# Kernel optimization log

Measured on AMD Instinct MI355X. Metric: run time of the kernel, lower is better.

## Reference

```python
import jax, jax.numpy as jnp
import numpy as np

B, C, H, W = 8, 512, 64, 64
TEMB = 512
HIDDEN = 1024  # int(C * prompt_hidden_ratio=2.0)
K = C // 2     # max(1, int(C * topk_ratio=0.5))


def silu(x):
    return x * jax.nn.sigmoid(x)


def conv1x1(h, w, b):
    # h: [b,c,hh,ww], w: [out,in], b: [out]
    return jnp.einsum('bchw,oc->bohw', h, w) + b[None, :, None, None]


def setup_inputs() -> dict:
    key = jax.random.key(0)
    ks = jax.random.split(key, 12)
    s = 0.02  # small init so softmax/attention stay well-conditioned
    return {
        'x': jax.random.normal(ks[0], (B, C, H, W), jnp.float32),
        'temb': jax.random.normal(ks[1], (B, TEMB), jnp.float32),
        'w_affine': jax.random.normal(ks[2], (2 * C, TEMB), jnp.float32) * s,
        'b_affine': jnp.zeros((2 * C,), jnp.float32),
        'w_tp': jax.random.normal(ks[3], (C, TEMB), jnp.float32) * s,
        'b_tp': jnp.zeros((C,), jnp.float32),
        'w_m1': jax.random.normal(ks[4], (HIDDEN, 2 * C), jnp.float32) * s,
        'b_m1': jnp.zeros((HIDDEN,), jnp.float32),
        'w_m2': jax.random.normal(ks[5], (C, HIDDEN), jnp.float32) * s,
        'b_m2': jnp.zeros((C,), jnp.float32),
        'wq': jax.random.normal(ks[6], (C, C), jnp.float32) * s,
        'bq': jnp.zeros((C,), jnp.float32),
        'wk': jax.random.normal(ks[7], (C, C), jnp.float32) * s,
        'bk': jnp.zeros((C,), jnp.float32),
        'wv': jax.random.normal(ks[8], (C, C), jnp.float32) * s,
        'bv': jnp.zeros((C,), jnp.float32),
        'wo': jax.random.normal(ks[9], (C, C), jnp.float32) * s,
        'bo': jnp.zeros((C,), jnp.float32),
    }


def reference(x, temb, w_affine, b_affine, w_tp, b_tp, w_m1, b_m1, w_m2, b_m2,
              wq, bq, wk, bk, wv, bv, wo, bo):
    b, c, hgt, wgt = x.shape
    hw = hgt * wgt

    # TimeScaleShift
    temb_act = silu(temb)
    ss = temb_act @ w_affine.T + b_affine              # [b, 2c]
    scale, shift = jnp.split(ss, 2, axis=1)
    h = x * (1.0 + scale[:, :, None, None]) + shift[:, :, None, None]

    # channel prompt
    gap = h.mean(axis=(2, 3))                          # [b, c]
    time_prompt = temb_act @ w_tp.T + b_tp             # [b, c]
    pm = jnp.concatenate([gap, time_prompt], axis=1)   # [b, 2c]
    prompt = silu(pm @ w_m1.T + b_m1) @ w_m2.T + b_m2  # [b, c]

    # top-k channel selection
    _, topk_idx = jax.lax.top_k(prompt, K)             # [b, K] int32

    # q/k/v 1x1 convs, then gather selected channels
    qf = conv1x1(h, wq, bq).reshape(b, c, hw)
    kf = conv1x1(h, wk, bk).reshape(b, c, hw)
    vf = conv1x1(h, wv, bv).reshape(b, c, hw)
    idx3 = topk_idx[:, :, None]
    q = jnp.take_along_axis(qf, idx3, axis=1)          # [b, K, hw]
    k_feat = jnp.take_along_axis(kf, idx3, axis=1)
    v = jnp.take_along_axis(vf, idx3, axis=1)

    # channel attention on the selected subset
    attn = jnp.einsum('bkn,bln->bkl', q, k_feat) * (K ** -0.5)  # [b, K, K]
    attn = jax.nn.softmax(attn, axis=2)
    out = jnp.einsum('bkl,bln->bkn', attn, v)                   # [b, K, hw]

    # scatter back into a zero tensor at the selected channels
    out_full = jax.vmap(
        lambda o, i: jnp.zeros((c, hw), o.dtype).at[i].set(o)
    )(out, topk_idx).reshape(b, c, hgt, wgt)

    return conv1x1(out_full, wo, bo)
```

## Files before the change

### kernel.cpp

```cpp
#include <hip/hip_runtime.h>
#include <hip/hip_bf16.h>
#include <math.h>

typedef __hip_bfloat16 bf16;
typedef __bf16 bf16x8 __attribute__((ext_vector_type(8)));
typedef float f32x4 __attribute__((ext_vector_type(4)));

static __device__ __forceinline__ float b2f(bf16 v) { return __bfloat162float(v); }
static __device__ __forceinline__ bf16 f2b(float v) { return __float2bfloat16(v); }

#define TM 128
#define TN 64
#define TK 32

template <typename TOUT>
__global__ __launch_bounds__(256) void gemm_bt(
    const bf16* __restrict__ A, size_t sA,
    const bf16* __restrict__ Bt, size_t sB,
    const float* __restrict__ bias, size_t sBias, int hasBias,
    TOUT* __restrict__ D, size_t sD,
    int M, int N, int Kd, int transStore)
{
    A  += (size_t)blockIdx.z * sA;
    Bt += (size_t)blockIdx.z * sB;
    D  += (size_t)blockIdx.z * sD;
    if (hasBias) bias += (size_t)blockIdx.z * sBias;

    const int m0 = blockIdx.y * TM, n0 = blockIdx.x * TN;
    const int t = threadIdx.x, wv = t >> 6, lane = t & 63;
    const int lr = lane & 15, quad = lane >> 4;

    __shared__ bf16 lA[TM][TK + 8];
    __shared__ bf16 lB[TN][TK + 8];

    f32x4 acc[2][4];
#pragma unroll
    for (int i = 0; i < 2; ++i)
#pragma unroll
        for (int j = 0; j < 4; ++j) acc[i][j] = (f32x4){0.f, 0.f, 0.f, 0.f};

    const int arow = t >> 1, acol = (t & 1) * 16;
    const int brow = t >> 2, bcol = (t & 3) * 8;
    const bf16* aptr = A  + (size_t)(m0 + arow) * Kd + acol;
    const bf16* bptr = Bt + (size_t)(n0 + brow) * Kd + bcol;

    for (int k0 = 0; k0 < Kd; k0 += TK) {
        __syncthreads();
        uint4 a0 = *(const uint4*)(aptr + k0);
        uint4 a1 = *(const uint4*)(aptr + k0 + 8);
        uint4 b0 = *(const uint4*)(bptr + k0);
        *(uint4*)(&lA[arow][acol])     = a0;
        *(uint4*)(&lA[arow][acol + 8]) = a1;
        *(uint4*)(&lB[brow][bcol])     = b0;
        __syncthreads();

        bf16x8 af0 = *(const bf16x8*)(&lA[wv * 32 + lr][quad * 8]);
        bf16x8 af1 = *(const bf16x8*)(&lA[wv * 32 + 16 + lr][quad * 8]);
#pragma unroll
        for (int j = 0; j < 4; ++j) {
            bf16x8 bfj = *(const bf16x8*)(&lB[j * 16 + lr][quad * 8]);
            acc[0][j] = __builtin_amdgcn_mfma_f32_16x16x32_bf16(af0, bfj, acc[0][j], 0, 0, 0);
            acc[1][j] = __builtin_amdgcn_mfma_f32_16x16x32_bf16(af1, bfj, acc[1][j], 0, 0, 0);
        }
    }

#pragma unroll
    for (int i = 0; i < 2; ++i) {
        const int mb = m0 + wv * 32 + i * 16 + quad * 4;
#pragma unroll
        for (int r = 0; r < 4; ++r) {
            const int mm = mb + r;
            const float bvv = hasBias ? bias[mm] : 0.f;
#pragma unroll
            for (int j = 0; j < 4; ++j) {
                const int nn = n0 + j * 16 + lr;
                const float v = acc[i][j][r] + bvv;
                const size_t o = transStore ? ((size_t)nn * M + mm)
                                            : ((size_t)mm * N + nn);
                if constexpr (__is_same(TOUT, float)) D[o] = v;
                else                                  D[o] = f2b(v);
            }
        }
    }
}

#define BROW 40

__global__ __launch_bounds__(256) void gemm_qkv(
    const bf16* __restrict__ Aall, const float* __restrict__ x,
    const float* __restrict__ ss, const float* __restrict__ bias,
    bf16* __restrict__ qb, bf16* __restrict__ kb, bf16* __restrict__ vT)
{
    const int b = blockIdx.z;
    const int m0 = blockIdx.y * 128;
    const int n0 = blockIdx.x * 64;
    const bf16* A = Aall + (size_t)b * 393216;
    bias += b * 768;

    const int t = threadIdx.x, wv = t >> 6, lane = t & 63;
    const int lr = lane & 15, quad = lane >> 4;

    __shared__ bf16 lA[3][128][TK + 8];
    __shared__ bf16 lBf[64 * BROW];

    f32x4 acc[3][2][4];
#pragma unroll
    for (int m = 0; m < 3; ++m)
#pragma unroll
        for (int i = 0; i < 2; ++i)
#pragma unroll
            for (int j = 0; j < 4; ++j) acc[m][i][j] = (f32x4){0.f, 0.f, 0.f, 0.f};

    const int arow = t >> 1, acol = (t & 1) * 16;
    const bf16* aptr = A + (size_t)(m0 + arow) * 512 + acol;
    const int kk = t >> 3;
    const int w8 = kk >> 3;
    const int nc = (t & 7) * 8;
    const float* xp0 = x + ((size_t)b * 512 + kk) * 4096 + n0 + nc;
    const float* ssp = ss + b * 1024 + kk;

    for (int k0 = 0; k0 < 512; k0 += TK) {
        __syncthreads();
        uint4 a[3][2];
#pragma unroll
        for (int m = 0; m < 3; ++m) {
            a[m][0] = *(const uint4*)(aptr + m * 131072 + k0);
            a[m][1] = *(const uint4*)(aptr + m * 131072 + k0 + 8);
        }
        const float4 f0 = *(const float4*)(xp0 + (size_t)k0 * 4096);
        const float4 f1 = *(const float4*)(xp0 + (size_t)k0 * 4096 + 4);
        const float sc = 1.f + ssp[k0];
        const float sh = ssp[512 + k0];
#pragma unroll
        for (int m = 0; m < 3; ++m) {
            *(uint4*)(&lA[m][arow][acol])     = a[m][0];
            *(uint4*)(&lA[m][arow][acol + 8]) = a[m][1];
        }
        {
            const float vals[8] = {f0.x, f0.y, f0.z, f0.w, f1.x, f1.y, f1.z, f1.w};
#pragma unroll
            for (int i = 0; i < 8; ++i) {
                const int n = nc + i;
                lBf[n * BROW + ((w8 ^ ((n >> 3) & 3)) << 3) + (kk & 7)] =
                    f2b(fmaf(vals[i], sc, sh));
            }
        }
        __syncthreads();

        bf16x8 af[3][2];
#pragma unroll
        for (int m = 0; m < 3; ++m) {
            af[m][0] = *(const bf16x8*)(&lA[m][wv * 32 + lr][quad * 8]);
            af[m][1] = *(const bf16x8*)(&lA[m][wv * 32 + 16 + lr][quad * 8]);
        }
#pragma unroll
        for (int j = 0; j < 4; ++j) {
            const int n = j * 16 + lr;
            bf16x8 bfj = *(const bf16x8*)(&lBf[n * BROW + ((quad ^ ((n >> 3) & 3)) << 3)]);
#pragma unroll
            for (int m = 0; m < 3; ++m) {
                acc[m][0][j] = __builtin_amdgcn_mfma_f32_16x16x32_bf16(af[m][0], bfj, acc[m][0][j], 0, 0, 0);
                acc[m][1][j] = __builtin_amdgcn_mfma_f32_16x16x32_bf16(af[m][1], bfj, acc[m][1][j], 0, 0, 0);
            }
        }
    }

#pragma unroll
    for (int m = 0; m < 3; ++m) {
#pragma unroll
        for (int i = 0; i < 2; ++i) {
            const int mb = m0 + wv * 32 + i * 16 + quad * 4;
#pragma unroll
            for (int r = 0; r < 4; ++r) {
                const int mm = mb + r;
                const float bvv = bias[m * 256 + mm];
#pragma unroll
                for (int j = 0; j < 4; ++j) {
                    const int nn = n0 + j * 16 + lr;
                    const float v = acc[m][i][j][r] + bvv;
                    if (m == 0)      qb[(size_t)b * 1048576 + (size_t)mm * 4096 + nn] = f2b(v);
                    else if (m == 1) kb[(size_t)b * 1048576 + (size_t)mm * 4096 + nn] = f2b(v);
                    else             vT[(size_t)b * 1048576 + (size_t)nn * 256 + mm] = f2b(v);
                }
            }
        }
    }
}

__global__ __launch_bounds__(256) void gemm_s_splitk(
    const bf16* __restrict__ qb, const bf16* __restrict__ kb,
    float* __restrict__ part)
{
    const int b = blockIdx.z >> 4, s = blockIdx.z & 15;
    const int m0 = blockIdx.y * TM, n0 = blockIdx.x * TN;
    const bf16* A  = qb + (size_t)b * 1048576;
    const bf16* Bt = kb + (size_t)b * 1048576;

    const int t = threadIdx.x, wv = t >> 6, lane = t & 63;
    const int lr = lane & 15, quad = lane >> 4;

    __shared__ bf16 lA[TM][TK + 8];
    __shared__ bf16 lB[TN][TK + 8];

    f32x4 acc[2][4];
#pragma unroll
    for (int i = 0; i < 2; ++i)
#pragma unroll
        for (int j = 0; j < 4; ++j) acc[i][j] = (f32x4){0.f, 0.f, 0.f, 0.f};

    const int arow = t >> 1, acol = (t & 1) * 16;
    const int brow = t >> 2, bcol = (t & 3) * 8;
    const bf16* aptr = A  + (size_t)(m0 + arow) * 4096 + acol;
    const bf16* bptr = Bt + (size_t)(n0 + brow) * 4096 + bcol;

    const int kBeg = s * 256, kEnd = kBeg + 256;
    for (int k0 = kBeg; k0 < kEnd; k0 += TK) {
        __syncthreads();
        uint4 a0 = *(const uint4*)(aptr + k0);
        uint4 a1 = *(const uint4*)(aptr + k0 + 8);
        uint4 b0 = *(const uint4*)(bptr + k0);
        *(uint4*)(&lA[arow][acol])     = a0;
        *(uint4*)(&lA[arow][acol + 8]) = a1;
        *(uint4*)(&lB[brow][bcol])     = b0;
        __syncthreads();

        bf16x8 af0 = *(const bf16x8*)(&lA[wv * 32 + lr][quad * 8]);
        bf16x8 af1 = *(const bf16x8*)(&lA[wv * 32 + 16 + lr][quad * 8]);
#pragma unroll
        for (int j = 0; j < 4; ++j) {
            bf16x8 bfj = *(const bf16x8*)(&lB[j * 16 + lr][quad * 8]);
            acc[0][j] = __builtin_amdgcn_mfma_f32_16x16x32_bf16(af0, bfj, acc[0][j], 0, 0, 0);
            acc[1][j] = __builtin_amdgcn_mfma_f32_16x16x32_bf16(af1, bfj, acc[1][j], 0, 0, 0);
        }
    }

    float* dst = part + ((size_t)(s * 8 + b) * 256) * 256;
#pragma unroll
    for (int i = 0; i < 2; ++i) {
        const int mb = m0 + wv * 32 + i * 16 + quad * 4;
#pragma unroll
        for (int r = 0; r < 4; ++r) {
            const int mm = mb + r;
#pragma unroll
            for (int j = 0; j < 4; ++j)
                dst[(size_t)mm * 256 + n0 + j * 16 + lr] = acc[i][j][r];
        }
    }
}


__global__ void k_silu(const float* __restrict__ in, float* __restrict__ out, int n)
{
    int i = blockIdx.x * 256 + threadIdx.x;
    if (i < n) {
        float v = in[i];
        out[i] = v / (1.f + expf(-v));
    }
}

__global__ void k_xmean(const float* __restrict__ x, float* __restrict__ xsum)
{
    const int bc = blockIdx.x;
    const float4* p = (const float4*)(x + (size_t)bc * 4096);
    float s = 0.f;
#pragma unroll
    for (int r = 0; r < 4; ++r) {
        float4 v = p[threadIdx.x + r * 256];
        s += v.x + v.y + v.z + v.w;
    }
    for (int off = 32; off; off >>= 1) s += __shfl_down(s, off);
    __shared__ float red[4];
    if ((threadIdx.x & 63) == 0) red[threadIdx.x >> 6] = s;
    __syncthreads();
    if (threadIdx.x == 0)
        xsum[bc] = red[0] + red[1] + red[2] + red[3];
}

__global__ void k_smallgemm(const float* __restrict__ in, const float* __restrict__ W,
                            const float* __restrict__ bias, float* __restrict__ out,
                            int Mrows, int O, int Kd, int act)
{
    const int gw = (blockIdx.x * 256 + threadIdx.x) >> 6;
    const int lane = threadIdx.x & 63;
    if (gw >= Mrows * O) return;
    const int m = gw / O, o = gw - m * O;
    float s = 0.f;
    for (int k = lane; k < Kd; k += 64)
        s += in[m * Kd + k] * W[(size_t)o * Kd + k];
    for (int off = 32; off; off >>= 1) s += __shfl_down(s, off);
    if (lane == 0) {
        s += bias[o];
        if (act) s = s / (1.f + expf(-s));
        out[m * O + o] = s;
    }
}

__global__ void k_mlp1(const float* __restrict__ ss, const float* __restrict__ xsum,
                       const float* __restrict__ tp, const float* __restrict__ w_m1,
                       const float* __restrict__ b_m1, float* __restrict__ hidden)
{
    const int gw = (blockIdx.x * 256 + threadIdx.x) >> 6;
    const int lane = threadIdx.x & 63;
    if (gw >= 8 * 1024) return;
    const int m = gw >> 10, o = gw & 1023;
    float s = 0.f;
    for (int k = lane; k < 1024; k += 64) {
        float pv;
        if (k < 512) pv = (1.f + ss[m * 1024 + k]) * (xsum[m * 512 + k] * (1.f / 4096.f))
                          + ss[m * 1024 + 512 + k];
        else         pv = tp[m * 512 + k - 512];
        s += pv * w_m1[(size_t)o * 1024 + k];
    }
    for (int off = 32; off; off >>= 1) s += __shfl_down(s, off);
    if (lane == 0) {
        s += b_m1[o];
        hidden[m * 1024 + o] = s / (1.f + expf(-s));
    }
}

__global__ void k_topk(const float* __restrict__ prompt, int* __restrict__ idx)
{
    __shared__ float v[512];
    __shared__ int sel[512];
    const int b = blockIdx.x, c = threadIdx.x;
    v[c] = prompt[b * 512 + c];
    __syncthreads();
    const float mv = v[c];
    int rank = 0;
    for (int j = 0; j < 512; ++j) {
        float o = v[j];
        rank += (o > mv) || (o == mv && j < c);
    }
    sel[c] = (rank < 256) ? 1 : 0;
    __syncthreads();
    if (rank < 256) {
        int pos = 0;
        for (int j = 0; j < c; ++j) pos += sel[j];
        idx[b * 256 + pos] = c;
    }
}

__global__ void k_gather(const int* __restrict__ idx,
                         const float* __restrict__ wq, const float* __restrict__ bq,
                         const float* __restrict__ wk, const float* __restrict__ bk,
                         const float* __restrict__ wv, const float* __restrict__ bv,
                         const float* __restrict__ wo,
                         bf16* __restrict__ wqkv_g, float* __restrict__ bqkv_g,
                         bf16* __restrict__ wo_g)
{
    const int b = blockIdx.z;
    const int* id = idx + b * 256;
    const int tid = blockIdx.x * 256 + threadIdx.x;
    {
        const int mat = tid >> 17, r = tid & 131071;
        const int j = r >> 9, c = r & 511;
        const int ch = id[j];
        const float* W = mat == 0 ? wq : (mat == 1 ? wk : wv);
        wqkv_g[(size_t)b * 393216 + tid] = f2b(W[ch * 512 + c]);
    }
    if (tid < 131072) {
        const int o = tid >> 8, j = tid & 255;
        wo_g[(size_t)b * 131072 + tid] = f2b(wo[o * 512 + id[j]]);
    }
    if (tid < 768) {
        const int m2 = tid >> 8, j = tid & 255;
        const float* Bv = m2 == 0 ? bq : (m2 == 1 ? bk : bv);
        bqkv_g[b * 768 + tid] = Bv[id[j]];
    }
}

__global__ void k_softmax_red(const float* __restrict__ part, bf16* __restrict__ Pt)
{
    const int row = blockIdx.x;
    const int b = row >> 8, j = row & 255;
    const int t = threadIdx.x;
    const int lane = t & 63, wv = t >> 6;
    __shared__ float redm[4], reds[4];
    float v = 0.f;
#pragma unroll
    for (int s = 0; s < 16; ++s)
        v += part[((size_t)(s * 8 + b) * 256 + j) * 256 + t];
    v *= 0.0625f;
    float m = v;
    for (int off = 32; off; off >>= 1) m = fmaxf(m, __shfl_down(m, off));
    if (lane == 0) redm[wv] = m;
    __syncthreads();
    m = fmaxf(fmaxf(redm[0], redm[1]), fmaxf(redm[2], redm[3]));
    const float e = __expf(v - m);
    float s = e;
    for (int off = 32; off; off >>= 1) s += __shfl_down(s, off);
    if (lane == 0) reds[wv] = s;
    __syncthreads();
    s = reds[0] + reds[1] + reds[2] + reds[3];
    Pt[(size_t)b * 65536 + (size_t)t * 256 + j] = f2b(e / s);
}


extern "C" void kernel_launch(void* const* d_in, const int* in_sizes, int n_in,
                              void* d_out, int out_size, void* d_ws, size_t ws_size,
                              hipStream_t stream)
{
    const float* x        = (const float*)d_in[0];
    const float* temb     = (const float*)d_in[1];
    const float* w_affine = (const float*)d_in[2];
    const float* b_affine = (const float*)d_in[3];
    const float* w_tp     = (const float*)d_in[4];
    const float* b_tp     = (const float*)d_in[5];
    const float* w_m1     = (const float*)d_in[6];
    const float* b_m1     = (const float*)d_in[7];
    const float* w_m2     = (const float*)d_in[8];
    const float* b_m2     = (const float*)d_in[9];
    const float* wq       = (const float*)d_in[10];
    const float* bq       = (const float*)d_in[11];
    const float* wk       = (const float*)d_in[12];
    const float* bk       = (const float*)d_in[13];
    const float* wv       = (const float*)d_in[14];
    const float* bv       = (const float*)d_in[15];
    const float* wo       = (const float*)d_in[16];
    const float* bo       = (const float*)d_in[17];
    float* out = (float*)d_out;

    char* ws = (char*)d_ws;
    size_t off = 0;
    auto alloc = [&](size_t bytes) -> char* {
        char* p = ws + off;
        off += (bytes + 255) & ~(size_t)255;
        return p;
    };

    float* temb_act = (float*)alloc(4096 * 4);
    float* ssb      = (float*)alloc(8192 * 4);
    float* tp       = (float*)alloc(4096 * 4);
    float* xsum     = (float*)alloc(4096 * 4);
    float* hidden   = (float*)alloc(8192 * 4);
    float* prompt   = (float*)alloc(4096 * 4);
    int*   idx      = (int*)alloc(2048 * 4);
    float* part   = (float*)alloc((size_t)16 * 8 * 256 * 256 * 4);
    bf16*  wqkv_g = (bf16*)alloc((size_t)8 * 768 * 512 * 2);
    float* bqkv_g = (float*)alloc(8 * 768 * 4);
    bf16*  wo_g   = (bf16*)alloc((size_t)8 * 512 * 256 * 2);
    bf16*  qb     = (bf16*)alloc((size_t)8 * 256 * 4096 * 2);
    bf16*  kb     = (bf16*)alloc((size_t)8 * 256 * 4096 * 2);
    bf16*  vT     = (bf16*)alloc((size_t)8 * 4096 * 256 * 2);
    bf16*  Pt     = (bf16*)alloc((size_t)8 * 256 * 256 * 2);
    bf16*  W2     = (bf16*)alloc((size_t)8 * 512 * 256 * 2);
    (void)ws_size; (void)n_in; (void)in_sizes; (void)out_size;

    k_silu<<<16, 256, 0, stream>>>(temb, temb_act, 4096);
    k_xmean<<<4096, 256, 0, stream>>>(x, xsum);
    k_smallgemm<<<2048, 256, 0, stream>>>(temb_act, w_affine, b_affine, ssb, 8, 1024, 512, 0);
    k_smallgemm<<<1024, 256, 0, stream>>>(temb_act, w_tp, b_tp, tp, 8, 512, 512, 0);
    k_mlp1<<<2048, 256, 0, stream>>>(ssb, xsum, tp, w_m1, b_m1, hidden);
    k_smallgemm<<<1024, 256, 0, stream>>>(hidden, w_m2, b_m2, prompt, 8, 512, 1024, 0);
    k_topk<<<8, 512, 0, stream>>>(prompt, idx);
    k_gather<<<dim3(1536, 1, 8), 256, 0, stream>>>(idx, wq, bq, wk, bk, wv, bv, wo,
                                                   wqkv_g, bqkv_g, wo_g);
    gemm_qkv<<<dim3(64, 2, 8), 256, 0, stream>>>(wqkv_g, x, ssb, bqkv_g, qb, kb, vT);
    gemm_s_splitk<<<dim3(4, 2, 128), 256, 0, stream>>>(qb, kb, part);
    k_softmax_red<<<2048, 256, 0, stream>>>(part, Pt);
    gemm_bt<bf16><<<dim3(4, 4, 8), 256, 0, stream>>>(wo_g, 131072, Pt, 65536,
                                                     nullptr, 0, 0,
                                                     W2, 131072, 512, 256, 256, 0);
    gemm_bt<float><<<dim3(64, 4, 8), 256, 0, stream>>>(W2, 131072, vT, 1048576,
                                                       bo, 0, 1,
                                                       out, 2097152, 512, 4096, 256, 0);
}
```

Measured before the change: 333.3 us.

## Reformulate channel attention via Gram matrix of x and folded weight products

Replaces the explicit q/k/v projections over all 4096 pixels with algebraic reassociation. It computes the symmetric Gram matrix x·xᵀ once per batch (upper-triangular tiles only), applies the scale/shift correction analytically, and forms the attention scores as Wq·G·Wkᵀ using hi/lo bf16 splitting for accuracy. The output path folds Wo·P·Wv·diag(1+scale) into one 512x512 matrix applied directly to x, with the shift and biases folded into a per-channel bias. This removes the large q/k/v intermediates and their HBM traffic, at the cost of more small kernels and possible bf16 precision loss in the Gram and fused weights.

```diff
diff --git a/kernel.cpp b/kernel.cpp
--- a/kernel.cpp
+++ b/kernel.cpp
@@ -8,30 +8,38 @@
 
 static __device__ __forceinline__ float b2f(bf16 v) { return __bfloat162float(v); }
 static __device__ __forceinline__ bf16 f2b(float v) { return __float2bfloat16(v); }
-
-#define TM 128
-#define TN 64
+static __device__ __forceinline__ unsigned int packbf(float a, float b)
+{
+    bf16 ha = f2b(a), hb = f2b(b);
+    unsigned short ua, ub;
+    __builtin_memcpy(&ua, &ha, 2);
+    __builtin_memcpy(&ub, &hb, 2);
+    return (unsigned int)ua | ((unsigned int)ub << 16);
+}
+
 #define TK 32
 
 template <typename TOUT>
 __global__ __launch_bounds__(256) void gemm_bt(
     const bf16* __restrict__ A, size_t sA,
     const bf16* __restrict__ Bt, size_t sB,
-    const float* __restrict__ bias, size_t sBias, int hasBias,
+    const float* __restrict__ bias, size_t sBias,
+    const float* __restrict__ colScale, size_t sCS,
     TOUT* __restrict__ D, size_t sD,
     int M, int N, int Kd, int transStore)
 {
     A  += (size_t)blockIdx.z * sA;
     Bt += (size_t)blockIdx.z * sB;
     D  += (size_t)blockIdx.z * sD;
-    if (hasBias) bias += (size_t)blockIdx.z * sBias;
-
-    const int m0 = blockIdx.y * TM, n0 = blockIdx.x * TN;
+    if (bias)     bias     += (size_t)blockIdx.z * sBias;
+    if (colScale) colScale += (size_t)blockIdx.z * sCS;
+
+    const int m0 = blockIdx.y * 128, n0 = blockIdx.x * 64;
     const int t = threadIdx.x, wv = t >> 6, lane = t & 63;
     const int lr = lane & 15, quad = lane >> 4;
 
-    __shared__ bf16 lA[TM][TK + 8];
-    __shared__ bf16 lB[TN][TK + 8];
+    __shared__ bf16 lA[128][TK + 8];
+    __shared__ bf16 lB[64][TK + 8];
 
     f32x4 acc[2][4];
 #pragma unroll
@@ -70,11 +78,12 @@
 #pragma unroll
         for (int r = 0; r < 4; ++r) {
             const int mm = mb + r;
-            const float bvv = hasBias ? bias[mm] : 0.f;
+            const float bvv = bias ? bias[mm] : 0.f;
 #pragma unroll
             for (int j = 0; j < 4; ++j) {
                 const int nn = n0 + j * 16 + lr;
-                const float v = acc[i][j][r] + bvv;
+                float v = acc[i][j][r] + bvv;
+                if (colScale) v *= (1.f + colScale[nn]);
                 const size_t o = transStore ? ((size_t)nn * M + mm)
                                             : ((size_t)mm * N + nn);
                 if constexpr (__is_same(TOUT, float)) D[o] = v;
@@ -84,123 +93,113 @@
     }
 }
 
-#define BROW 40
-
-__global__ __launch_bounds__(256) void gemm_qkv(
-    const bf16* __restrict__ Aall, const float* __restrict__ x,
-    const float* __restrict__ ss, const float* __restrict__ bias,
-    bf16* __restrict__ qb, bf16* __restrict__ kb, bf16* __restrict__ vT)
-{
-    const int b = blockIdx.z;
-    const int m0 = blockIdx.y * 128;
-    const int n0 = blockIdx.x * 64;
-    const bf16* A = Aall + (size_t)b * 393216;
-    bias += b * 768;
-
+__global__ __launch_bounds__(256) void gemm_bt2(
+    const bf16* __restrict__ A1, const bf16* __restrict__ A2, size_t sA,
+    const bf16* __restrict__ B1, const bf16* __restrict__ B2, size_t sB,
+    bf16* __restrict__ Dhi, bf16* __restrict__ Dlo,
+    float* __restrict__ Df, size_t sD,
+    int M, int N, int Kd, int transStore)
+{
+    A1 += (size_t)blockIdx.z * sA;
+    A2 += (size_t)blockIdx.z * sA;
+    B1 += (size_t)blockIdx.z * sB;
+    B2 += (size_t)blockIdx.z * sB;
+
+    const int m0 = blockIdx.y * 128, n0 = blockIdx.x * 64;
     const int t = threadIdx.x, wv = t >> 6, lane = t & 63;
     const int lr = lane & 15, quad = lane >> 4;
 
-    __shared__ bf16 lA[3][128][TK + 8];
-    __shared__ bf16 lBf[64 * BROW];
-
-    f32x4 acc[3][2][4];
-#pragma unroll
-    for (int m = 0; m < 3; ++m)
-#pragma unroll
-        for (int i = 0; i < 2; ++i)
-#pragma unroll
-            for (int j = 0; j < 4; ++j) acc[m][i][j] = (f32x4){0.f, 0.f, 0.f, 0.f};
+    __shared__ bf16 lA1[128][TK + 8];
+    __shared__ bf16 lA2[128][TK + 8];
+    __shared__ bf16 lB1[64][TK + 8];
+    __shared__ bf16 lB2[64][TK + 8];
+
+    f32x4 acc[2][4];
+#pragma unroll
+    for (int i = 0; i < 2; ++i)
+#pragma unroll
+        for (int j = 0; j < 4; ++j) acc[i][j] = (f32x4){0.f, 0.f, 0.f, 0.f};
 
     const int arow = t >> 1, acol = (t & 1) * 16;
-    const bf16* aptr = A + (size_t)(m0 + arow) * 512 + acol;
-    const int kk = t >> 3;
-    const int w8 = kk >> 3;
-    const int nc = (t & 7) * 8;
-    const float* xp0 = x + ((size_t)b * 512 + kk) * 4096 + n0 + nc;
-    const float* ssp = ss + b * 1024 + kk;
-
-    for (int k0 = 0; k0 < 512; k0 += TK) {
-        __syncthreads();
-        uint4 a[3][2];
-#pragma unroll
-        for (int m = 0; m < 3; ++m) {
-            a[m][0] = *(const uint4*)(aptr + m * 131072 + k0);
-            a[m][1] = *(const uint4*)(aptr + m * 131072 + k0 + 8);
-        }
-        const float4 f0 = *(const float4*)(xp0 + (size_t)k0 * 4096);
-        const float4 f1 = *(const float4*)(xp0 + (size_t)k0 * 4096 + 4);
-        const float sc = 1.f + ssp[k0];
-        const float sh = ssp[512 + k0];
-#pragma unroll
-        for (int m = 0; m < 3; ++m) {
-            *(uint4*)(&lA[m][arow][acol])     = a[m][0];
-            *(uint4*)(&lA[m][arow][acol + 8]) = a[m][1];
-        }
-        {
-            const float vals[8] = {f0.x, f0.y, f0.z, f0.w, f1.x, f1.y, f1.z, f1.w};
-#pragma unroll
-            for (int i = 0; i < 8; ++i) {
-                const int n = nc + i;
-                lBf[n * BROW + ((w8 ^ ((n >> 3) & 3)) << 3) + (kk & 7)] =
-                    f2b(fmaf(vals[i], sc, sh));
-            }
-        }
-        __syncthreads();
-
-        bf16x8 af[3][2];
-#pragma unroll
-        for (int m = 0; m < 3; ++m) {
-            af[m][0] = *(const bf16x8*)(&lA[m][wv * 32 + lr][quad * 8]);
-            af[m][1] = *(const bf16x8*)(&lA[m][wv * 32 + 16 + lr][quad * 8]);
-        }
+    const int brow = t >> 2, bcol = (t & 3) * 8;
+    const size_t aoff = (size_t)(m0 + arow) * Kd + acol;
+    const size_t boff = (size_t)(n0 + brow) * Kd + bcol;
+
+    for (int k0 = 0; k0 < Kd; k0 += TK) {
+        __syncthreads();
+        uint4 a10 = *(const uint4*)(A1 + aoff + k0);
+        uint4 a11 = *(const uint4*)(A1 + aoff + k0 + 8);
+        uint4 a20 = *(const uint4*)(A2 + aoff + k0);
+        uint4 a21 = *(const uint4*)(A2 + aoff + k0 + 8);
+        uint4 b1  = *(const uint4*)(B1 + boff + k0);
+        uint4 b2  = *(const uint4*)(B2 + boff + k0);
+        *(uint4*)(&lA1[arow][acol])     = a10;
+        *(uint4*)(&lA1[arow][acol + 8]) = a11;
+        *(uint4*)(&lA2[arow][acol])     = a20;
+        *(uint4*)(&lA2[arow][acol + 8]) = a21;
+        *(uint4*)(&lB1[brow][bcol])     = b1;
+        *(uint4*)(&lB2[brow][bcol])     = b2;
+        __syncthreads();
+
+        bf16x8 a1f0 = *(const bf16x8*)(&lA1[wv * 32 + lr][quad * 8]);
+        bf16x8 a1f1 = *(const bf16x8*)(&lA1[wv * 32 + 16 + lr][quad * 8]);
+        bf16x8 a2f0 = *(const bf16x8*)(&lA2[wv * 32 + lr][quad * 8]);
+        bf16x8 a2f1 = *(const bf16x8*)(&lA2[wv * 32 + 16 + lr][quad * 8]);
 #pragma unroll
         for (int j = 0; j < 4; ++j) {
-            const int n = j * 16 + lr;
-            bf16x8 bfj = *(const bf16x8*)(&lBf[n * BROW + ((quad ^ ((n >> 3) & 3)) << 3)]);
-#pragma unroll
-            for (int m = 0; m < 3; ++m) {
-                acc[m][0][j] = __builtin_amdgcn_mfma_f32_16x16x32_bf16(af[m][0], bfj, acc[m][0][j], 0, 0, 0);
-                acc[m][1][j] = __builtin_amdgcn_mfma_f32_16x16x32_bf16(af[m][1], bfj, acc[m][1][j], 0, 0, 0);
-            }
-        }
-    }
-
-#pragma unroll
-    for (int m = 0; m < 3; ++m) {
-#pragma unroll
-        for (int i = 0; i < 2; ++i) {
-            const int mb = m0 + wv * 32 + i * 16 + quad * 4;
-#pragma unroll
-            for (int r = 0; r < 4; ++r) {
-                const int mm = mb + r;
-                const float bvv = bias[m * 256 + mm];
-#pragma unroll
-                for (int j = 0; j < 4; ++j) {
-                    const int nn = n0 + j * 16 + lr;
-                    const float v = acc[m][i][j][r] + bvv;
-                    if (m == 0)      qb[(size_t)b * 1048576 + (size_t)mm * 4096 + nn] = f2b(v);
-                    else if (m == 1) kb[(size_t)b * 1048576 + (size_t)mm * 4096 + nn] = f2b(v);
-                    else             vT[(size_t)b * 1048576 + (size_t)nn * 256 + mm] = f2b(v);
+            bf16x8 b1j = *(const bf16x8*)(&lB1[j * 16 + lr][quad * 8]);
+            bf16x8 b2j = *(const bf16x8*)(&lB2[j * 16 + lr][quad * 8]);
+            acc[0][j] = __builtin_amdgcn_mfma_f32_16x16x32_bf16(a1f0, b1j, acc[0][j], 0, 0, 0);
+            acc[0][j] = __builtin_amdgcn_mfma_f32_16x16x32_bf16(a2f0, b2j, acc[0][j], 0, 0, 0);
+            acc[1][j] = __builtin_amdgcn_mfma_f32_16x16x32_bf16(a1f1, b1j, acc[1][j], 0, 0, 0);
+            acc[1][j] = __builtin_amdgcn_mfma_f32_16x16x32_bf16(a2f1, b2j, acc[1][j], 0, 0, 0);
+        }
+    }
+
+#pragma unroll
+    for (int i = 0; i < 2; ++i) {
+        const int mb = m0 + wv * 32 + i * 16 + quad * 4;
+#pragma unroll
+        for (int r = 0; r < 4; ++r) {
+            const int mm = mb + r;
+#pragma unroll
+            for (int j = 0; j < 4; ++j) {
+                const int nn = n0 + j * 16 + lr;
+                const float v = acc[i][j][r];
+                const size_t o = (transStore ? ((size_t)nn * M + mm)
+                                             : ((size_t)mm * N + nn))
+                                 + (size_t)blockIdx.z * sD;
+                if (Df) {
+                    Df[o] = v;
+                } else {
+                    bf16 h = f2b(v);
+                    Dhi[o] = h;
+                    Dlo[o] = f2b(v - b2f(h));
                 }
             }
         }
     }
 }
 
-__global__ __launch_bounds__(256) void gemm_s_splitk(
-    const bf16* __restrict__ qb, const bf16* __restrict__ kb,
-    float* __restrict__ part)
-{
-    const int b = blockIdx.z >> 4, s = blockIdx.z & 15;
-    const int m0 = blockIdx.y * TM, n0 = blockIdx.x * TN;
-    const bf16* A  = qb + (size_t)b * 1048576;
-    const bf16* Bt = kb + (size_t)b * 1048576;
+__global__ __launch_bounds__(256) void gemm_gram(
+    const float* __restrict__ x, float* __restrict__ part)
+{
+    const int li = blockIdx.x, s = blockIdx.y, b = blockIdx.z;
+    int mi, ni;
+    if (li < 8)       { mi = 0; ni = li; }
+    else if (li < 14) { mi = 1; ni = li - 6; }
+    else if (li < 18) { mi = 2; ni = li - 10; }
+    else              { mi = 3; ni = li - 12; }
+    const int m0 = mi * 128, n0 = ni * 64;
+    const float* xb = x + (size_t)b * 512 * 4096;
 
     const int t = threadIdx.x, wv = t >> 6, lane = t & 63;
     const int lr = lane & 15, quad = lane >> 4;
 
-    __shared__ bf16 lA[TM][TK + 8];
-    __shared__ bf16 lB[TN][TK + 8];
+    __shared__ bf16 lA[128][TK + 8];
+    __shared__ bf16 lB[64][TK + 8];
+    unsigned int* lAu = (unsigned int*)lA;
+    unsigned int* lBu = (unsigned int*)lB;
 
     f32x4 acc[2][4];
 #pragma unroll
@@ -210,18 +209,30 @@
 
     const int arow = t >> 1, acol = (t & 1) * 16;
     const int brow = t >> 2, bcol = (t & 3) * 8;
-    const bf16* aptr = A  + (size_t)(m0 + arow) * 4096 + acol;
-    const bf16* bptr = Bt + (size_t)(n0 + brow) * 4096 + bcol;
-
-    const int kBeg = s * 256, kEnd = kBeg + 256;
+    const float* aptr = xb + (size_t)(m0 + arow) * 4096 + acol;
+    const float* bptr = xb + (size_t)(n0 + brow) * 4096 + bcol;
+
+    const int kBeg = s * 1024, kEnd = kBeg + 1024;
     for (int k0 = kBeg; k0 < kEnd; k0 += TK) {
         __syncthreads();
-        uint4 a0 = *(const uint4*)(aptr + k0);
-        uint4 a1 = *(const uint4*)(aptr + k0 + 8);
-        uint4 b0 = *(const uint4*)(bptr + k0);
-        *(uint4*)(&lA[arow][acol])     = a0;
-        *(uint4*)(&lA[arow][acol + 8]) = a1;
-        *(uint4*)(&lB[brow][bcol])     = b0;
+        float4 af[4], bf[2];
+#pragma unroll
+        for (int q = 0; q < 4; ++q) af[q] = *(const float4*)(aptr + k0 + q * 4);
+#pragma unroll
+        for (int q = 0; q < 2; ++q) bf[q] = *(const float4*)(bptr + k0 + q * 4);
+        {
+            unsigned int w[8];
+            const float* fa = (const float*)af;
+#pragma unroll
+            for (int q = 0; q < 8; ++q) w[q] = packbf(fa[2 * q], fa[2 * q + 1]);
+            *(uint4*)&lAu[arow * 20 + acol / 2]     = *(uint4*)&w[0];
+            *(uint4*)&lAu[arow * 20 + acol / 2 + 4] = *(uint4*)&w[4];
+            unsigned int v[4];
+            const float* fb = (const float*)bf;
+#pragma unroll
+            for (int q = 0; q < 4; ++q) v[q] = packbf(fb[2 * q], fb[2 * q + 1]);
+            *(uint4*)&lBu[brow * 20 + bcol / 2] = *(uint4*)&v[0];
+        }
         __syncthreads();
 
         bf16x8 af0 = *(const bf16x8*)(&lA[wv * 32 + lr][quad * 8]);
@@ -234,7 +245,7 @@
         }
     }
 
-    float* dst = part + ((size_t)(s * 8 + b) * 256) * 256;
+    float* dst = part + ((size_t)(s * 8 + b)) * 262144;
 #pragma unroll
     for (int i = 0; i < 2; ++i) {
         const int mb = m0 + wv * 32 + i * 16 + quad * 4;
@@ -243,7 +254,104 @@
             const int mm = mb + r;
 #pragma unroll
             for (int j = 0; j < 4; ++j)
-                dst[(size_t)mm * 256 + n0 + j * 16 + lr] = acc[i][j][r];
+                dst[(size_t)mm * 512 + n0 + j * 16 + lr] = acc[i][j][r];
+        }
+    }
+}
+
+__global__ void k_fixG(const float* __restrict__ part, const float* __restrict__ ss,
+                       const float* __restrict__ xsum,
+                       bf16* __restrict__ Ghi, bf16* __restrict__ Glo)
+{
+    const int e = blockIdx.x * 256 + threadIdx.x;
+    const int b = e >> 18, rem = e & 262143;
+    const int c1 = rem >> 9, c2 = rem & 511;
+    const int stored = (c2 >> 6) >= 2 * (c1 >> 7);
+    const size_t src = stored ? ((size_t)c1 * 512 + c2) : ((size_t)c2 * 512 + c1);
+    float gx = 0.f;
+#pragma unroll
+    for (int s = 0; s < 4; ++s)
+        gx += part[((size_t)(s * 8 + b)) * 262144 + src];
+    const float s1 = ss[b * 1024 + c1], sh1 = ss[b * 1024 + 512 + c1];
+    const float s2 = ss[b * 1024 + c2], sh2 = ss[b * 1024 + 512 + c2];
+    const float xs1 = xsum[b * 512 + c1], xs2 = xsum[b * 512 + c2];
+    const float g = (1.f + s1) * (1.f + s2) * gx + (1.f + s1) * sh2 * xs1
+                    + sh1 * (1.f + s2) * xs2 + 4096.f * sh1 * sh2;
+    const bf16 h = f2b(g);
+    Ghi[e] = h;
+    Glo[e] = f2b(g - b2f(h));
+}
+
+__global__ __launch_bounds__(256) void gemm_final(
+    const bf16* __restrict__ W3p, const float* __restrict__ x,
+    const float* __restrict__ bias2, float* __restrict__ out)
+{
+    const int b = blockIdx.z;
+    const int m0 = blockIdx.y * 128, n0 = blockIdx.x * 64;
+    const bf16* A = W3p + (size_t)b * 262144;
+    const float* xb = x + (size_t)b * 512 * 4096;
+    bias2 += b * 512;
+    out += (size_t)b * 2097152;
+
+    const int t = threadIdx.x, wv = t >> 6, lane = t & 63;
+    const int lr = lane & 15, quad = lane >> 4;
+
+    __shared__ bf16 lA[128][TK + 8];
+    __shared__ unsigned int lBu[64 * 20];
+
+    f32x4 acc[2][4];
+#pragma unroll
+    for (int i = 0; i < 2; ++i)
+#pragma unroll
+        for (int j = 0; j < 4; ++j) acc[i][j] = (f32x4){0.f, 0.f, 0.f, 0.f};
+
+    const int arow = t >> 1, acol = (t & 1) * 16;
+    const bf16* aptr = A + (size_t)(m0 + arow) * 512 + acol;
+    const int kp = t >> 4, nc = (t & 15) * 4;
+    const int grp = kp >> 2, wIn = kp & 3;
+    const float* xp0 = xb + (size_t)(2 * kp) * 4096 + n0 + nc;
+
+    for (int k0 = 0; k0 < 512; k0 += TK) {
+        __syncthreads();
+        uint4 a0 = *(const uint4*)(aptr + k0);
+        uint4 a1 = *(const uint4*)(aptr + k0 + 8);
+        const float4 r0 = *(const float4*)(xp0 + (size_t)k0 * 4096);
+        const float4 r1 = *(const float4*)(xp0 + (size_t)k0 * 4096 + 4096);
+        *(uint4*)(&lA[arow][acol])     = a0;
+        *(uint4*)(&lA[arow][acol + 8]) = a1;
+        {
+            const float v0[4] = {r0.x, r0.y, r0.z, r0.w};
+            const float v1[4] = {r1.x, r1.y, r1.z, r1.w};
+#pragma unroll
+            for (int i = 0; i < 4; ++i) {
+                const int n = nc + i;
+                lBu[n * 20 + (((grp ^ ((n >> 3) & 3)) << 2) | wIn)] =
+                    packbf(v0[i], v1[i]);
+            }
+        }
+        __syncthreads();
+
+        bf16x8 af0 = *(const bf16x8*)(&lA[wv * 32 + lr][quad * 8]);
+        bf16x8 af1 = *(const bf16x8*)(&lA[wv * 32 + 16 + lr][quad * 8]);
+#pragma unroll
+        for (int j = 0; j < 4; ++j) {
+            const int n = j * 16 + lr;
+            bf16x8 bfj = *(const bf16x8*)(&lBu[n * 20 + ((quad ^ ((n >> 3) & 3)) << 2)]);
+            acc[0][j] = __builtin_amdgcn_mfma_f32_16x16x32_bf16(af0, bfj, acc[0][j], 0, 0, 0);
+            acc[1][j] = __builtin_amdgcn_mfma_f32_16x16x32_bf16(af1, bfj, acc[1][j], 0, 0, 0);
+        }
+    }
+
+#pragma unroll
+    for (int i = 0; i < 2; ++i) {
+        const int mb = m0 + wv * 32 + i * 16 + quad * 4;
+#pragma unroll
+        for (int r = 0; r < 4; ++r) {
+            const int mm = mb + r;
+            const float bvv = bias2[mm];
+#pragma unroll
+            for (int j = 0; j < 4; ++j)
+                out[(size_t)mm * 4096 + n0 + j * 16 + lr] = acc[i][j][r] + bvv;
         }
     }
 }
@@ -345,41 +453,96 @@
                          const float* __restrict__ wk, const float* __restrict__ bk,
                          const float* __restrict__ wv, const float* __restrict__ bv,
                          const float* __restrict__ wo,
-                         bf16* __restrict__ wqkv_g, float* __restrict__ bqkv_g,
-                         bf16* __restrict__ wo_g)
+                         bf16* __restrict__ wq_g, bf16* __restrict__ wk_g,
+                         bf16* __restrict__ wo_g, bf16* __restrict__ wvT_g,
+                         float* __restrict__ bq_g, float* __restrict__ bk_g,
+                         float* __restrict__ bv_g)
 {
     const int b = blockIdx.z;
     const int* id = idx + b * 256;
     const int tid = blockIdx.x * 256 + threadIdx.x;
     {
-        const int mat = tid >> 17, r = tid & 131071;
-        const int j = r >> 9, c = r & 511;
+        const int j = tid >> 9, c = tid & 511;
         const int ch = id[j];
-        const float* W = mat == 0 ? wq : (mat == 1 ? wk : wv);
-        wqkv_g[(size_t)b * 393216 + tid] = f2b(W[ch * 512 + c]);
-    }
-    if (tid < 131072) {
+        wq_g[(size_t)b * 131072 + tid] = f2b(wq[ch * 512 + c]);
+        wk_g[(size_t)b * 131072 + tid] = f2b(wk[ch * 512 + c]);
+    }
+    {
         const int o = tid >> 8, j = tid & 255;
         wo_g[(size_t)b * 131072 + tid] = f2b(wo[o * 512 + id[j]]);
     }
-    if (tid < 768) {
-        const int m2 = tid >> 8, j = tid & 255;
-        const float* Bv = m2 == 0 ? bq : (m2 == 1 ? bk : bv);
-        bqkv_g[b * 768 + tid] = Bv[id[j]];
-    }
-}
-
-__global__ void k_softmax_red(const float* __restrict__ part, bf16* __restrict__ Pt)
+    {
+        const int c = tid >> 8, l = tid & 255;
+        wvT_g[(size_t)b * 131072 + tid] = f2b(wv[id[l] * 512 + c]);
+    }
+    if (tid < 256) {
+        const int ch = id[tid];
+        bq_g[b * 256 + tid] = bq[ch];
+        bk_g[b * 256 + tid] = bk[ch];
+        bv_g[b * 256 + tid] = bv[ch];
+    }
+}
+
+__global__ void k_qhkh(const bf16* __restrict__ wq_g, const bf16* __restrict__ wk_g,
+                       const float* __restrict__ ss, const float* __restrict__ xsum,
+                       float* __restrict__ qh, float* __restrict__ kh)
+{
+    const int gw = (blockIdx.x * 256 + threadIdx.x) >> 6;
+    const int lane = threadIdx.x & 63;
+    const int b = gw >> 9, rem = gw & 511;
+    const int which = rem >> 8, j = rem & 255;
+    const bf16* W = which ? wk_g : wq_g;
+    float s = 0.f;
+    for (int c = lane; c < 512; c += 64) {
+        const float hs = (1.f + ss[b * 1024 + c]) * xsum[b * 512 + c]
+                         + 4096.f * ss[b * 1024 + 512 + c];
+        s += b2f(W[(size_t)b * 131072 + j * 512 + c]) * hs;
+    }
+    for (int off = 32; off; off >>= 1) s += __shfl_down(s, off);
+    if (lane == 0) (which ? kh : qh)[b * 256 + j] = s;
+}
+
+__global__ void k_vsh(const float* __restrict__ wv, const int* __restrict__ idx,
+                      const float* __restrict__ ss, float* __restrict__ vsh)
+{
+    const int gw = (blockIdx.x * 256 + threadIdx.x) >> 6;
+    const int lane = threadIdx.x & 63;
+    const int b = gw >> 8, l = gw & 255;
+    const int ch = idx[b * 256 + l];
+    float s = 0.f;
+    for (int c = lane; c < 512; c += 64)
+        s += wv[ch * 512 + c] * ss[b * 1024 + 512 + c];
+    for (int off = 32; off; off >>= 1) s += __shfl_down(s, off);
+    if (lane == 0) vsh[b * 256 + l] = s;
+}
+
+__global__ void k_bias2(const bf16* __restrict__ W2, const float* __restrict__ vsh,
+                        const float* __restrict__ bv_g, const float* __restrict__ bo,
+                        float* __restrict__ bias2)
+{
+    const int gw = (blockIdx.x * 256 + threadIdx.x) >> 6;
+    const int lane = threadIdx.x & 63;
+    const int b = gw >> 9, o = gw & 511;
+    float s = 0.f;
+    for (int l = lane; l < 256; l += 64)
+        s += b2f(W2[(size_t)b * 131072 + o * 256 + l]) * (vsh[b * 256 + l] + bv_g[b * 256 + l]);
+    for (int off = 32; off; off >>= 1) s += __shfl_down(s, off);
+    if (lane == 0) bias2[b * 512 + o] = s + bo[o];
+}
+
+__global__ void k_softmax2(const float* __restrict__ S, const float* __restrict__ qh,
+                           const float* __restrict__ kh, const float* __restrict__ bq_g,
+                           const float* __restrict__ bk_g, bf16* __restrict__ Pt)
 {
     const int row = blockIdx.x;
     const int b = row >> 8, j = row & 255;
     const int t = threadIdx.x;
     const int lane = t & 63, wv = t >> 6;
     __shared__ float redm[4], reds[4];
-    float v = 0.f;
-#pragma unroll
-    for (int s = 0; s < 16; ++s)
-        v += part[((size_t)(s * 8 + b) * 256 + j) * 256 + t];
+    float v = S[(size_t)row * 256 + t]
+            + bq_g[b * 256 + j] * kh[b * 256 + t]
+            + bk_g[b * 256 + t] * qh[b * 256 + j]
+            + 4096.f * bq_g[b * 256 + j] * bk_g[b * 256 + t];
     v *= 0.0625f;
     float m = v;
     for (int off = 32; off; off >>= 1) m = fmaxf(m, __shfl_down(m, off));
@@ -435,17 +598,29 @@
     float* hidden   = (float*)alloc(8192 * 4);
     float* prompt   = (float*)alloc(4096 * 4);
     int*   idx      = (int*)alloc(2048 * 4);
-    float* part   = (float*)alloc((size_t)16 * 8 * 256 * 256 * 4);
-    bf16*  wqkv_g = (bf16*)alloc((size_t)8 * 768 * 512 * 2);
-    float* bqkv_g = (float*)alloc(8 * 768 * 4);
+    float* part   = (float*)alloc((size_t)4 * 8 * 512 * 512 * 4);
+    bf16*  Ghi    = (bf16*)alloc((size_t)8 * 512 * 512 * 2);
+    bf16*  Glo    = (bf16*)alloc((size_t)8 * 512 * 512 * 2);
+    bf16*  wq_g   = (bf16*)alloc((size_t)8 * 256 * 512 * 2);
+    bf16*  wk_g   = (bf16*)alloc((size_t)8 * 256 * 512 * 2);
     bf16*  wo_g   = (bf16*)alloc((size_t)8 * 512 * 256 * 2);
-    bf16*  qb     = (bf16*)alloc((size_t)8 * 256 * 4096 * 2);
-    bf16*  kb     = (bf16*)alloc((size_t)8 * 256 * 4096 * 2);
-    bf16*  vT     = (bf16*)alloc((size_t)8 * 4096 * 256 * 2);
+    bf16*  wvT_g  = (bf16*)alloc((size_t)8 * 512 * 256 * 2);
+    float* bq_g   = (float*)alloc(8 * 256 * 4);
+    float* bk_g   = (float*)alloc(8 * 256 * 4);
+    float* bv_g   = (float*)alloc(8 * 256 * 4);
+    bf16*  Tt_hi  = (bf16*)alloc((size_t)8 * 256 * 512 * 2);
+    bf16*  Tt_lo  = (bf16*)alloc((size_t)8 * 256 * 512 * 2);
+    float* Sbuf   = (float*)alloc((size_t)8 * 256 * 256 * 4);
+    float* qh     = (float*)alloc(2048 * 4);
+    float* kh     = (float*)alloc(2048 * 4);
+    float* vsh    = (float*)alloc(2048 * 4);
     bf16*  Pt     = (bf16*)alloc((size_t)8 * 256 * 256 * 2);
     bf16*  W2     = (bf16*)alloc((size_t)8 * 512 * 256 * 2);
+    float* bias2  = (float*)alloc(4096 * 4);
+    bf16*  W3p    = (bf16*)alloc((size_t)8 * 512 * 512 * 2);
     (void)ws_size; (void)n_in; (void)in_sizes; (void)out_size;
 
+    gemm_gram<<<dim3(20, 4, 8), 256, 0, stream>>>(x, part);
     k_silu<<<16, 256, 0, stream>>>(temb, temb_act, 4096);
     k_xmean<<<4096, 256, 0, stream>>>(x, xsum);
     k_smallgemm<<<2048, 256, 0, stream>>>(temb_act, w_affine, b_affine, ssb, 8, 1024, 512, 0);
@@ -453,15 +628,25 @@
     k_mlp1<<<2048, 256, 0, stream>>>(ssb, xsum, tp, w_m1, b_m1, hidden);
     k_smallgemm<<<1024, 256, 0, stream>>>(hidden, w_m2, b_m2, prompt, 8, 512, 1024, 0);
     k_topk<<<8, 512, 0, stream>>>(prompt, idx);
-    k_gather<<<dim3(1536, 1, 8), 256, 0, stream>>>(idx, wq, bq, wk, bk, wv, bv, wo,
-                                                   wqkv_g, bqkv_g, wo_g);
-    gemm_qkv<<<dim3(64, 2, 8), 256, 0, stream>>>(wqkv_g, x, ssb, bqkv_g, qb, kb, vT);
-    gemm_s_splitk<<<dim3(4, 2, 128), 256, 0, stream>>>(qb, kb, part);
-    k_softmax_red<<<2048, 256, 0, stream>>>(part, Pt);
+    k_gather<<<dim3(512, 1, 8), 256, 0, stream>>>(idx, wq, bq, wk, bk, wv, bv, wo,
+                                                  wq_g, wk_g, wo_g, wvT_g,
+                                                  bq_g, bk_g, bv_g);
+    k_fixG<<<8192, 256, 0, stream>>>(part, ssb, xsum, Ghi, Glo);
+    gemm_bt2<<<dim3(4, 4, 8), 256, 0, stream>>>(Ghi, Glo, 262144, wk_g, wk_g, 131072,
+                                                Tt_hi, Tt_lo, nullptr, 131072,
+                                                512, 256, 512, 1);
+    gemm_bt2<<<dim3(4, 2, 8), 256, 0, stream>>>(wq_g, wq_g, 131072, Tt_hi, Tt_lo, 131072,
+                                                nullptr, nullptr, Sbuf, 65536,
+                                                256, 256, 512, 0);
+    k_qhkh<<<1024, 256, 0, stream>>>(wq_g, wk_g, ssb, xsum, qh, kh);
+    k_vsh<<<512, 256, 0, stream>>>(wv, idx, ssb, vsh);
+    k_softmax2<<<2048, 256, 0, stream>>>(Sbuf, qh, kh, bq_g, bk_g, Pt);
     gemm_bt<bf16><<<dim3(4, 4, 8), 256, 0, stream>>>(wo_g, 131072, Pt, 65536,
-                                                     nullptr, 0, 0,
+                                                     nullptr, 0, nullptr, 0,
                                                      W2, 131072, 512, 256, 256, 0);
-    gemm_bt<float><<<dim3(64, 4, 8), 256, 0, stream>>>(W2, 131072, vT, 1048576,
-                                                       bo, 0, 1,
-                                                       out, 2097152, 512, 4096, 256, 0);
-}
+    k_bias2<<<1024, 256, 0, stream>>>(W2, vsh, bv_g, bo, bias2);
+    gemm_bt<bf16><<<dim3(8, 4, 8), 256, 0, stream>>>(W2, 131072, wvT_g, 131072,
+                                                     nullptr, 0, ssb, 1024,
+                                                     W3p, 262144, 512, 512, 256, 0);
+    gemm_final<<<dim3(64, 4, 8), 256, 0, stream>>>(W3p, x, bias2, out);
+}
```

Result: slower. 414.8 us (+24.5%).
